# Optimization experiments

Hardware: AMD Instinct MI355X
Metric: run time of the kernel (lower is better)

Reference implementation:

```python
import jax, jax.numpy as jnp
import numpy as np

INPUT_DIM = 1024
OUTPUT_DIM = 1024
NUM_EXPERTS = 8
HIDDEN_DIM = 64
N_TOKENS = 8192


def setup_inputs() -> dict:
    key = jax.random.key(0)
    ks = jax.random.split(key, 7)
    s_in = 1.0 / np.sqrt(INPUT_DIM)
    s_h = 1.0 / np.sqrt(HIDDEN_DIM)
    return {
        "x": jax.random.normal(ks[0], (N_TOKENS, INPUT_DIM), dtype=jnp.float32),
        # per-expert Linear(input_dim, output_dim): weight [E, out, in], bias [E, out]
        "We": jax.random.uniform(ks[1], (NUM_EXPERTS, OUTPUT_DIM, INPUT_DIM), minval=-s_in, maxval=s_in, dtype=jnp.float32),
        "be": jax.random.uniform(ks[2], (NUM_EXPERTS, OUTPUT_DIM), minval=-s_in, maxval=s_in, dtype=jnp.float32),
        # gating: Linear(input_dim, hidden) -> ReLU -> Linear(hidden, num_experts)
        "Wg1": jax.random.uniform(ks[3], (HIDDEN_DIM, INPUT_DIM), minval=-s_in, maxval=s_in, dtype=jnp.float32),
        "bg1": jax.random.uniform(ks[4], (HIDDEN_DIM,), minval=-s_in, maxval=s_in, dtype=jnp.float32),
        "Wg2": jax.random.uniform(ks[5], (NUM_EXPERTS, HIDDEN_DIM), minval=-s_h, maxval=s_h, dtype=jnp.float32),
        "bg2": jax.random.uniform(ks[6], (NUM_EXPERTS,), minval=-s_h, maxval=s_h, dtype=jnp.float32),
    }


def reference(x, We, be, Wg1, bg1, Wg2, bg2):
    # gating network
    h = jax.nn.relu(x @ Wg1.T + bg1)                 # [N, H]
    gate_scores = h @ Wg2.T + bg2                    # [N, E]
    gate_weights = jax.nn.softmax(gate_scores, axis=-1)
    top2_weights, top2_indices = jax.lax.top_k(gate_weights, 2)  # [N, 2]
    # dense expert compute: every expert on every token (faithful to source)
    expert_outputs = jnp.einsum('ni,eoi->neo', x, We) + be       # [N, E, D_out]
    # gather top-2 expert outputs and combine
    gathered = jnp.take_along_axis(expert_outputs, top2_indices[:, :, None], axis=1)  # [N, 2, D_out]
    output = jnp.sum(gathered * top2_weights[:, :, None], axis=1)  # [N, D_out]
    return output, gate_weights, top2_indices
```

## Files before the change

### kernel.cpp

```cpp
#include <hip/hip_runtime.h>
#include <stdint.h>

#define N_TOKENS 8192
#define IN_DIM   1024
#define OUT_DIM  1024
#define NE       8
#define HID      64

typedef __attribute__((ext_vector_type(8))) short bf16x8;
typedef __attribute__((ext_vector_type(4))) float f32x4;

__device__ __forceinline__ unsigned short f2bf(float f) {
    unsigned int b = __float_as_uint(f);
    b += 0x7fffu + ((b >> 16) & 1u);
    return (unsigned short)(b >> 16);
}

__device__ __forceinline__ void gl16(const unsigned short* g, unsigned short* l) {
    __builtin_amdgcn_global_load_lds(
        (const __attribute__((address_space(1))) unsigned int*)g,
        (__attribute__((address_space(3))) unsigned int*)l,
        16, 0, 0);
}

__global__ __launch_bounds__(256) void conv_bf16(
    const float* __restrict__ src, unsigned short* __restrict__ dst, int n4)
{
    int i = blockIdx.x * 256 + threadIdx.x;
    const int stride = gridDim.x * 256;
    for (; i < n4; i += stride) {
        float4 v = ((const float4*)src)[i];
        ushort4 h;
        h.x = f2bf(v.x); h.y = f2bf(v.y); h.z = f2bf(v.z); h.w = f2bf(v.w);
        ((ushort4*)dst)[i] = h;
    }
}

__global__ __launch_bounds__(256) void gating_kernel(
    const float* __restrict__ x, const float* __restrict__ Wg1, const float* __restrict__ bg1,
    const float* __restrict__ Wg2, const float* __restrict__ bg2,
    float* __restrict__ out_gw, float* __restrict__ out_idx,
    int* __restrict__ counts, int* __restrict__ bucket_tok, float* __restrict__ bucket_w)
{
    __shared__ float Xs[32][68];
    __shared__ float Gs[32][68];
    __shared__ float Hs[64][65];
    __shared__ float W2s[NE][HID];
    __shared__ float b2s[NE];

    const int tid = threadIdx.x;
    const int t0  = blockIdx.x * 64;

    for (int i = tid; i < NE * HID; i += 256) W2s[i >> 6][i & 63] = Wg2[i];
    if (tid < NE) b2s[tid] = bg2[tid];

    const int ty = tid >> 4, tx = tid & 15;
    float acc[4][4] = {};

    const int sr  = tid >> 2;
    const int skq = tid & 3;
    const float* xsrc = x   + (size_t)(t0 + sr) * IN_DIM + skq * 8;
    const float* gsrc = Wg1 + (size_t)sr        * IN_DIM + skq * 8;

    for (int k0 = 0; k0 < IN_DIM; k0 += 32) {
        __syncthreads();
        float4 v0 = *(const float4*)(xsrc + k0);
        float4 v1 = *(const float4*)(xsrc + k0 + 4);
        float4 w0 = *(const float4*)(gsrc + k0);
        float4 w1 = *(const float4*)(gsrc + k0 + 4);
        Xs[skq*8+0][sr]=v0.x; Xs[skq*8+1][sr]=v0.y; Xs[skq*8+2][sr]=v0.z; Xs[skq*8+3][sr]=v0.w;
        Xs[skq*8+4][sr]=v1.x; Xs[skq*8+5][sr]=v1.y; Xs[skq*8+6][sr]=v1.z; Xs[skq*8+7][sr]=v1.w;
        Gs[skq*8+0][sr]=w0.x; Gs[skq*8+1][sr]=w0.y; Gs[skq*8+2][sr]=w0.z; Gs[skq*8+3][sr]=w0.w;
        Gs[skq*8+4][sr]=w1.x; Gs[skq*8+5][sr]=w1.y; Gs[skq*8+6][sr]=w1.z; Gs[skq*8+7][sr]=w1.w;
        __syncthreads();
#pragma unroll
        for (int kk = 0; kk < 32; ++kk) {
            float4 a = *(const float4*)&Xs[kk][ty * 4];
            float4 b = *(const float4*)&Gs[kk][tx * 4];
            acc[0][0] += a.x*b.x; acc[0][1] += a.x*b.y; acc[0][2] += a.x*b.z; acc[0][3] += a.x*b.w;
            acc[1][0] += a.y*b.x; acc[1][1] += a.y*b.y; acc[1][2] += a.y*b.z; acc[1][3] += a.y*b.w;
            acc[2][0] += a.z*b.x; acc[2][1] += a.z*b.y; acc[2][2] += a.z*b.z; acc[2][3] += a.z*b.w;
            acc[3][0] += a.w*b.x; acc[3][1] += a.w*b.y; acc[3][2] += a.w*b.z; acc[3][3] += a.w*b.w;
        }
    }

    float bg[4];
#pragma unroll
    for (int j = 0; j < 4; ++j) bg[j] = bg1[tx * 4 + j];
#pragma unroll
    for (int i = 0; i < 4; ++i)
#pragma unroll
        for (int j = 0; j < 4; ++j)
            Hs[ty * 4 + i][tx * 4 + j] = fmaxf(acc[i][j] + bg[j], 0.0f);
    __syncthreads();

    if (tid < 64) {
        const int token = t0 + tid;
        float sc[NE];
#pragma unroll
        for (int e2 = 0; e2 < NE; ++e2) {
            float s = b2s[e2];
#pragma unroll
            for (int j = 0; j < HID; ++j) s += Hs[tid][j] * W2s[e2][j];
            sc[e2] = s;
        }
        float m = sc[0];
#pragma unroll
        for (int e2 = 1; e2 < NE; ++e2) m = fmaxf(m, sc[e2]);
        float sum = 0.0f;
#pragma unroll
        for (int e2 = 0; e2 < NE; ++e2) { sc[e2] = expf(sc[e2] - m); sum += sc[e2]; }
        const float inv = 1.0f / sum;
#pragma unroll
        for (int e2 = 0; e2 < NE; ++e2) { sc[e2] *= inv; out_gw[(size_t)token * NE + e2] = sc[e2]; }

        int i1 = 0; float v1 = sc[0];
#pragma unroll
        for (int e2 = 1; e2 < NE; ++e2) if (sc[e2] > v1) { v1 = sc[e2]; i1 = e2; }
        int i2 = -1; float v2 = -1e30f;
#pragma unroll
        for (int e2 = 0; e2 < NE; ++e2) {
            if (e2 == i1) continue;
            if (i2 < 0 || sc[e2] > v2) { v2 = sc[e2]; i2 = e2; }
        }
        out_idx[(size_t)token * 2 + 0] = (float)i1;
        out_idx[(size_t)token * 2 + 1] = (float)i2;

        const unsigned long long lmask = (1ull << tid) - 1ull;
#pragma unroll
        for (int e2 = 0; e2 < NE; ++e2) {
            unsigned long long m1 = __ballot(i1 == e2);
            unsigned long long m2 = __ballot(i2 == e2);
            int c1 = __popcll(m1), c2 = __popcll(m2);
            int base = 0;
            if (tid == 0 && (c1 + c2) > 0) base = atomicAdd(&counts[e2 * 16], c1 + c2);
            base = __shfl(base, 0);
            if (i1 == e2) {
                int pos = base + __popcll(m1 & lmask);
                bucket_tok[e2 * N_TOKENS + pos] = token * 2 + 0;
                bucket_w  [e2 * N_TOKENS + pos] = v1;
            }
            if (i2 == e2) {
                int pos = base + c1 + __popcll(m2 & lmask);
                bucket_tok[e2 * N_TOKENS + pos] = token * 2 + 1;
                bucket_w  [e2 * N_TOKENS + pos] = v2;
            }
        }
    }
}

#define BM 128
#define KS 32

__global__ __launch_bounds__(256) void expert_gemm(
    const unsigned short* __restrict__ xh, const unsigned short* __restrict__ wh,
    const float* __restrict__ be, const int* __restrict__ counts,
    const int* __restrict__ bucket_tok, const float* __restrict__ bucket_w,
    float* __restrict__ tmp)
{
    const int e  = blockIdx.z;
    const int tt = blockIdx.y;
    const int ot = blockIdx.x;
    const int cnt = counts[e * 16];
    if (tt * BM >= cnt) return;

    __shared__ unsigned short Xh[BM * KS], Wh[BM * KS];
    __shared__ int   slt[BM];
    __shared__ float wts[BM];

    const int tid  = threadIdx.x;
    const int wv   = tid >> 6;
    const int lane = tid & 63;

    if (tid < BM) {
        int idx = tt * BM + tid;
        slt[tid] = (idx < cnt) ? bucket_tok[e * N_TOKENS + idx] : -1;
        wts[tid] = (idx < cnt) ? bucket_w [e * N_TOKENS + idx] : 0.0f;
    }
    __syncthreads();

    const int l4 = lane >> 2;
    const int kq = lane & 3;
    const int rA = wv * 32 + l4;
    const int s0 = slt[rA], s1 = slt[rA + 16];
    const int tk0 = (s0 < 0) ? 0 : (s0 >> 1);
    const int tk1 = (s1 < 0) ? 0 : (s1 >> 1);

    const unsigned short* sX0 = xh + (size_t)tk0 * IN_DIM + kq * 8;
    const unsigned short* sX1 = xh + (size_t)tk1 * IN_DIM + kq * 8;
    const unsigned short* sW0 = wh + ((size_t)e * OUT_DIM + ot * BM + rA) * IN_DIM + kq * 8;
    const unsigned short* sW1 = sW0 + (size_t)16 * IN_DIM;

    unsigned short* dX = &Xh[wv * 1024];
    unsigned short* dW = &Wh[wv * 1024];

    const int wm = wv >> 1, wn = wv & 1;
    const int fr = lane & 15;
    const int kb = (lane >> 4) * 8;

    f32x4 acc[4][4];
#pragma unroll
    for (int mi = 0; mi < 4; ++mi)
#pragma unroll
        for (int ni = 0; ni < 4; ++ni) acc[mi][ni] = (f32x4)0.0f;

    for (int k0 = 0; k0 < IN_DIM; k0 += KS) {
        __syncthreads();
        gl16(sX0 + k0, dX);  gl16(sX1 + k0, dX + 512);
        gl16(sW0 + k0, dW);  gl16(sW1 + k0, dW + 512);
        __syncthreads();

        bf16x8 ah[4], bh[4];
#pragma unroll
        for (int mi = 0; mi < 4; ++mi)
            ah[mi] = *(const bf16x8*)&Xh[(wm * 64 + mi * 16 + fr) * KS + kb];
#pragma unroll
        for (int ni = 0; ni < 4; ++ni)
            bh[ni] = *(const bf16x8*)&Wh[(wn * 64 + ni * 16 + fr) * KS + kb];
#pragma unroll
        for (int mi = 0; mi < 4; ++mi)
#pragma unroll
            for (int ni = 0; ni < 4; ++ni)
                acc[mi][ni] = __builtin_amdgcn_mfma_f32_16x16x32_bf16(ah[mi], bh[ni], acc[mi][ni], 0, 0, 0);
    }

    const int colbase = ot * BM + wn * 64;
    float bias[4];
#pragma unroll
    for (int ni = 0; ni < 4; ++ni) bias[ni] = be[(size_t)e * OUT_DIM + colbase + ni * 16 + fr];

#pragma unroll
    for (int mi = 0; mi < 4; ++mi) {
#pragma unroll
        for (int r = 0; r < 4; ++r) {
            const int ri = wm * 64 + mi * 16 + (lane >> 4) * 4 + r;
            const int s  = slt[ri];
            if (s < 0) continue;
            const float w = wts[ri];
            float* orow = tmp + (size_t)s * OUT_DIM + colbase;
#pragma unroll
            for (int ni = 0; ni < 4; ++ni)
                orow[ni * 16 + fr] = w * (acc[mi][ni][r] + bias[ni]);
        }
    }
}

__global__ __launch_bounds__(256) void combine_kernel(
    const float* __restrict__ tmp, float* __restrict__ out, int n4)
{
    int i = blockIdx.x * 256 + threadIdx.x;
    const int stride = gridDim.x * 256;
    const int row4 = OUT_DIM / 4;
    for (; i < n4; i += stride) {
        int t  = i / row4;
        int d4 = i - t * row4;
        float4 a = ((const float4*)tmp)[(size_t)(2 * t)     * row4 + d4];
        float4 b = ((const float4*)tmp)[(size_t)(2 * t + 1) * row4 + d4];
        float4 o;
        o.x = a.x + b.x; o.y = a.y + b.y; o.z = a.z + b.z; o.w = a.w + b.w;
        ((float4*)out)[i] = o;
    }
}

extern "C" void kernel_launch(void* const* d_in, const int* in_sizes, int n_in,
                              void* d_out, int out_size, void* d_ws, size_t ws_size,
                              hipStream_t stream) {
    const float* x   = (const float*)d_in[0];
    const float* We  = (const float*)d_in[1];
    const float* be  = (const float*)d_in[2];
    const float* Wg1 = (const float*)d_in[3];
    const float* bg1 = (const float*)d_in[4];
    const float* Wg2 = (const float*)d_in[5];
    const float* bg2 = (const float*)d_in[6];

    float* out     = (float*)d_out;
    float* out_gw  = out + (size_t)N_TOKENS * OUT_DIM;
    float* out_idx = out_gw + (size_t)N_TOKENS * NE;

    char* ws = (char*)d_ws;
    int*   counts = (int*)ws;
    int*   btok   = (int*)(ws + 1024);
    float* bw     = (float*)(ws + 1024 + 262144);
    unsigned short* xh = (unsigned short*)(ws + 525312);
    unsigned short* wh = xh + (size_t)N_TOKENS * IN_DIM;
    float* tmp = (float*)(wh + (size_t)NE * OUT_DIM * IN_DIM);

    hipMemsetAsync(counts, 0, 1024, stream);

    conv_bf16<<<1024, 256, 0, stream>>>(x,  xh, (N_TOKENS * IN_DIM) / 4);
    conv_bf16<<<1024, 256, 0, stream>>>(We, wh, (NE * OUT_DIM * IN_DIM) / 4);

    gating_kernel<<<N_TOKENS / 64, 256, 0, stream>>>(
        x, Wg1, bg1, Wg2, bg2, out_gw, out_idx, counts, btok, bw);

    dim3 grid(OUT_DIM / BM, N_TOKENS / BM, NE);
    expert_gemm<<<grid, 256, 0, stream>>>(xh, wh, be, counts, btok, bw, tmp);

    combine_kernel<<<2048, 256, 0, stream>>>(tmp, out, (N_TOKENS * OUT_DIM) / 4);
}
```

Measured before the change: 258.6 us.

## Use split-bf16 MFMA for gating GEMM and fuse x bf16 conversion into it

The gating first-layer GEMM moves from scalar FP32 FMAs to bf16 MFMA instructions. It uses a hi/lo split (three MFMAs per tile) so accuracy stays close to fp32, which matters because top-2 selection is sensitive to small errors. The separate conversion pass of x to bf16 is removed; the gating kernel writes the bf16 x for the expert GEMM as it streams x. Wg1 is pre-split by a small kernel, and tiles are loaded into LDS via global_load_lds. Residual split error could still flip top-k ties relative to fp32.

```diff
diff --git a/kernel.cpp b/kernel.cpp
--- a/kernel.cpp
+++ b/kernel.cpp
@@ -14,6 +14,9 @@
     unsigned int b = __float_as_uint(f);
     b += 0x7fffu + ((b >> 16) & 1u);
     return (unsigned short)(b >> 16);
+}
+__device__ __forceinline__ float bf2f(unsigned short u) {
+    return __uint_as_float(((unsigned int)u) << 16);
 }
 
 __device__ __forceinline__ void gl16(const unsigned short* g, unsigned short* l) {
@@ -36,62 +39,101 @@
     }
 }
 
+__global__ __launch_bounds__(256) void split_wg1(
+    const float* __restrict__ src, unsigned short* __restrict__ hi,
+    unsigned short* __restrict__ lo, int n4)
+{
+    int i = blockIdx.x * 256 + threadIdx.x;
+    if (i >= n4) return;
+    float4 v = ((const float4*)src)[i];
+    ushort4 h, l;
+    h.x = f2bf(v.x); l.x = f2bf(v.x - bf2f(h.x));
+    h.y = f2bf(v.y); l.y = f2bf(v.y - bf2f(h.y));
+    h.z = f2bf(v.z); l.z = f2bf(v.z - bf2f(h.z));
+    h.w = f2bf(v.w); l.w = f2bf(v.w - bf2f(h.w));
+    ((ushort4*)hi)[i] = h;
+    ((ushort4*)lo)[i] = l;
+}
+
 __global__ __launch_bounds__(256) void gating_kernel(
-    const float* __restrict__ x, const float* __restrict__ Wg1, const float* __restrict__ bg1,
+    const float* __restrict__ x, unsigned short* __restrict__ xh_out,
+    const unsigned short* __restrict__ wg1h, const unsigned short* __restrict__ wg1l,
+    const float* __restrict__ bg1,
     const float* __restrict__ Wg2, const float* __restrict__ bg2,
     float* __restrict__ out_gw, float* __restrict__ out_idx,
     int* __restrict__ counts, int* __restrict__ bucket_tok, float* __restrict__ bucket_w)
 {
-    __shared__ float Xs[32][68];
-    __shared__ float Gs[32][68];
-    __shared__ float Hs[64][65];
+    __shared__ unsigned short Xh_s[64 * 32], Xl_s[64 * 32];
+    __shared__ unsigned short Gh_s[64 * 32], Gl_s[64 * 32];
+    __shared__ float Hs[64][68];
     __shared__ float W2s[NE][HID];
     __shared__ float b2s[NE];
 
-    const int tid = threadIdx.x;
-    const int t0  = blockIdx.x * 64;
+    const int tid  = threadIdx.x;
+    const int wv   = tid >> 6;
+    const int lane = tid & 63;
+    const int t0   = blockIdx.x * 64;
 
     for (int i = tid; i < NE * HID; i += 256) W2s[i >> 6][i & 63] = Wg2[i];
     if (tid < NE) b2s[tid] = bg2[tid];
 
-    const int ty = tid >> 4, tx = tid & 15;
-    float acc[4][4] = {};
-
-    const int sr  = tid >> 2;
-    const int skq = tid & 3;
-    const float* xsrc = x   + (size_t)(t0 + sr) * IN_DIM + skq * 8;
-    const float* gsrc = Wg1 + (size_t)sr        * IN_DIM + skq * 8;
+    const int r = tid >> 2;
+    const int c = tid & 3;
+    const float* xsrc = x + (size_t)(t0 + r) * IN_DIM + c * 8;
+    unsigned short* xdst = xh_out + (size_t)(t0 + r) * IN_DIM + c * 8;
+
+    const unsigned short* gh_src = wg1h + (size_t)(wv * 16 + (lane >> 2)) * IN_DIM + (lane & 3) * 8;
+    const unsigned short* gl_src = wg1l + (size_t)(wv * 16 + (lane >> 2)) * IN_DIM + (lane & 3) * 8;
+    unsigned short* gh_dst = &Gh_s[wv * 512];
+    unsigned short* gl_dst = &Gl_s[wv * 512];
+
+    const int fr = lane & 15;
+    const int kb = (lane >> 4) * 8;
+
+    f32x4 acc[4];
+#pragma unroll
+    for (int mi = 0; mi < 4; ++mi) acc[mi] = (f32x4)0.0f;
 
     for (int k0 = 0; k0 < IN_DIM; k0 += 32) {
-        __syncthreads();
         float4 v0 = *(const float4*)(xsrc + k0);
         float4 v1 = *(const float4*)(xsrc + k0 + 4);
-        float4 w0 = *(const float4*)(gsrc + k0);
-        float4 w1 = *(const float4*)(gsrc + k0 + 4);
-        Xs[skq*8+0][sr]=v0.x; Xs[skq*8+1][sr]=v0.y; Xs[skq*8+2][sr]=v0.z; Xs[skq*8+3][sr]=v0.w;
-        Xs[skq*8+4][sr]=v1.x; Xs[skq*8+5][sr]=v1.y; Xs[skq*8+6][sr]=v1.z; Xs[skq*8+7][sr]=v1.w;
-        Gs[skq*8+0][sr]=w0.x; Gs[skq*8+1][sr]=w0.y; Gs[skq*8+2][sr]=w0.z; Gs[skq*8+3][sr]=w0.w;
-        Gs[skq*8+4][sr]=w1.x; Gs[skq*8+5][sr]=w1.y; Gs[skq*8+6][sr]=w1.z; Gs[skq*8+7][sr]=w1.w;
+        bf16x8 xh8, xl8;
+        {
+            float vv[8] = {v0.x, v0.y, v0.z, v0.w, v1.x, v1.y, v1.z, v1.w};
+#pragma unroll
+            for (int j = 0; j < 8; ++j) {
+                unsigned short h = f2bf(vv[j]);
+                xh8[j] = (short)h;
+                xl8[j] = (short)f2bf(vv[j] - bf2f(h));
+            }
+        }
+        *(bf16x8*)(xdst + k0) = xh8;
+
         __syncthreads();
-#pragma unroll
-        for (int kk = 0; kk < 32; ++kk) {
-            float4 a = *(const float4*)&Xs[kk][ty * 4];
-            float4 b = *(const float4*)&Gs[kk][tx * 4];
-            acc[0][0] += a.x*b.x; acc[0][1] += a.x*b.y; acc[0][2] += a.x*b.z; acc[0][3] += a.x*b.w;
-            acc[1][0] += a.y*b.x; acc[1][1] += a.y*b.y; acc[1][2] += a.y*b.z; acc[1][3] += a.y*b.w;
-            acc[2][0] += a.z*b.x; acc[2][1] += a.z*b.y; acc[2][2] += a.z*b.z; acc[2][3] += a.z*b.w;
-            acc[3][0] += a.w*b.x; acc[3][1] += a.w*b.y; acc[3][2] += a.w*b.z; acc[3][3] += a.w*b.w;
-        }
-    }
-
-    float bg[4];
-#pragma unroll
-    for (int j = 0; j < 4; ++j) bg[j] = bg1[tx * 4 + j];
-#pragma unroll
-    for (int i = 0; i < 4; ++i)
-#pragma unroll
-        for (int j = 0; j < 4; ++j)
-            Hs[ty * 4 + i][tx * 4 + j] = fmaxf(acc[i][j] + bg[j], 0.0f);
+        *(bf16x8*)&Xh_s[r * 32 + c * 8] = xh8;
+        *(bf16x8*)&Xl_s[r * 32 + c * 8] = xl8;
+        gl16(gh_src + k0, gh_dst);
+        gl16(gl_src + k0, gl_dst);
+        __syncthreads();
+
+        bf16x8 bh = *(const bf16x8*)&Gh_s[(wv * 16 + fr) * 32 + kb];
+        bf16x8 bl = *(const bf16x8*)&Gl_s[(wv * 16 + fr) * 32 + kb];
+#pragma unroll
+        for (int mi = 0; mi < 4; ++mi) {
+            bf16x8 ah = *(const bf16x8*)&Xh_s[(mi * 16 + fr) * 32 + kb];
+            bf16x8 al = *(const bf16x8*)&Xl_s[(mi * 16 + fr) * 32 + kb];
+            acc[mi] = __builtin_amdgcn_mfma_f32_16x16x32_bf16(ah, bh, acc[mi], 0, 0, 0);
+            acc[mi] = __builtin_amdgcn_mfma_f32_16x16x32_bf16(ah, bl, acc[mi], 0, 0, 0);
+            acc[mi] = __builtin_amdgcn_mfma_f32_16x16x32_bf16(al, bh, acc[mi], 0, 0, 0);
+        }
+    }
+
+    const float bgv = bg1[wv * 16 + fr];
+#pragma unroll
+    for (int mi = 0; mi < 4; ++mi)
+#pragma unroll
+        for (int rg = 0; rg < 4; ++rg)
+            Hs[mi * 16 + (lane >> 4) * 4 + rg][wv * 16 + fr] = fmaxf(acc[mi][rg] + bgv, 0.0f);
     __syncthreads();
 
     if (tid < 64) {
@@ -281,17 +323,19 @@
     int*   counts = (int*)ws;
     int*   btok   = (int*)(ws + 1024);
     float* bw     = (float*)(ws + 1024 + 262144);
-    unsigned short* xh = (unsigned short*)(ws + 525312);
-    unsigned short* wh = xh + (size_t)N_TOKENS * IN_DIM;
-    float* tmp = (float*)(wh + (size_t)NE * OUT_DIM * IN_DIM);
+    unsigned short* xh   = (unsigned short*)(ws + 525312);
+    unsigned short* wh   = xh + (size_t)N_TOKENS * IN_DIM;
+    unsigned short* wg1h = wh + (size_t)NE * OUT_DIM * IN_DIM;
+    unsigned short* wg1l = wg1h + (size_t)HID * IN_DIM;
+    float* tmp = (float*)(wg1l + (size_t)HID * IN_DIM);
 
     hipMemsetAsync(counts, 0, 1024, stream);
 
-    conv_bf16<<<1024, 256, 0, stream>>>(x,  xh, (N_TOKENS * IN_DIM) / 4);
+    split_wg1<<<64, 256, 0, stream>>>(Wg1, wg1h, wg1l, (HID * IN_DIM) / 4);
     conv_bf16<<<1024, 256, 0, stream>>>(We, wh, (NE * OUT_DIM * IN_DIM) / 4);
 
     gating_kernel<<<N_TOKENS / 64, 256, 0, stream>>>(
-        x, Wg1, bg1, Wg2, bg2, out_gw, out_idx, counts, btok, bw);
+        x, xh, wg1h, wg1l, bg1, Wg2, bg2, out_gw, out_idx, counts, btok, bw);
 
     dim3 grid(OUT_DIM / BM, N_TOKENS / BM, NE);
     expert_gemm<<<grid, 256, 0, stream>>>(xh, wh, be, counts, btok, bw, tmp);
```

After: 237.1 us. 8.3% less time.
